# Kernel optimization log

Hardware: AMD Instinct MI355X
Metric: run time of the kernel (lower is better)

The kernel has to match this reference:

```python
import jax, jax.numpy as jnp
import numpy as np

HIDDEN = 32
SEQ = 1440
IN = 11


def lstm_layer(x, Wih, Whh, bih, bhh):
    # x: (B, T, I); PyTorch gate order i, f, g, o stacked along first dim of W (4H, I)
    B, T, _ = x.shape
    H = Whh.shape[1]
    xg = jnp.einsum('bti,gi->btg', x, Wih) + bih + bhh  # (B, T, 4H) input projections precomputed

    def step(carry, xg_t):
        h, c = carry
        g = xg_t + h @ Whh.T  # (B, 4H)
        i, f, gg, o = jnp.split(g, 4, axis=-1)
        i = jax.nn.sigmoid(i)
        f = jax.nn.sigmoid(f)
        gg = jnp.tanh(gg)
        o = jax.nn.sigmoid(o)
        c = f * c + i * gg
        h = o * jnp.tanh(c)
        return (h, c), h

    h0 = jnp.zeros((B, H), x.dtype)
    (_, _), hs = jax.lax.scan(step, (h0, h0), jnp.swapaxes(xg, 0, 1))  # hs: (T, B, H)
    return jnp.swapaxes(hs, 0, 1)


def setup_inputs() -> dict:
    key = jax.random.key(0)
    ks = jax.random.split(key, 14)
    s = 0.1
    return {
        'x': jax.random.normal(ks[0], (1024, IN, SEQ), dtype=jnp.float32),
        'Wih0': jax.random.normal(ks[1], (4 * HIDDEN, IN), dtype=jnp.float32) * s,
        'Whh0': jax.random.normal(ks[2], (4 * HIDDEN, HIDDEN), dtype=jnp.float32) * s,
        'bih0': jax.random.normal(ks[3], (4 * HIDDEN,), dtype=jnp.float32) * s,
        'bhh0': jax.random.normal(ks[4], (4 * HIDDEN,), dtype=jnp.float32) * s,
        'Wih1': jax.random.normal(ks[5], (4 * HIDDEN, HIDDEN), dtype=jnp.float32) * s,
        'Whh1': jax.random.normal(ks[6], (4 * HIDDEN, HIDDEN), dtype=jnp.float32) * s,
        'bih1': jax.random.normal(ks[7], (4 * HIDDEN,), dtype=jnp.float32) * s,
        'bhh1': jax.random.normal(ks[8], (4 * HIDDEN,), dtype=jnp.float32) * s,
        'fc1_w': jax.random.normal(ks[9], (16, HIDDEN), dtype=jnp.float32) * s,
        'fc1_b': jax.random.normal(ks[10], (16,), dtype=jnp.float32) * s,
        'fc2_w': jax.random.normal(ks[11], (1, 16), dtype=jnp.float32) * s,
        'fc2_b': jax.random.normal(ks[12], (1,), dtype=jnp.float32) * s,
    }


def reference(x, Wih0, Whh0, bih0, bhh0, Wih1, Whh1, bih1, bhh1, fc1_w, fc1_b, fc2_w, fc2_b):
    # x.view(-1, 11, 1440).transpose(1, 2) -> (B, 1440, 11)
    xt = jnp.swapaxes(x.reshape(-1, IN, SEQ), 1, 2)
    h1 = lstm_layer(xt, Wih0, Whh0, bih0, bhh0)
    h2 = lstm_layer(h1, Wih1, Whh1, bih1, bhh1)
    out = h2[:, :SEQ - 1, :]  # out[:, -1440:-1, :] with T=1440 -> steps 0..1438
    out = jnp.tanh(out @ fc1_w.T + fc1_b)
    out = out @ fc2_w.T + fc2_b
    return out.squeeze(-1)  # (B, 1439)
```

## Files before the change

### kernel.cpp

```cpp
#include <hip/hip_runtime.h>

#define H    32
#define SEQ  1440
#define NT   (SEQ - 1)
#define INP  11
#define TC   64

__device__ __forceinline__ float rcp_fast(float x) { return __builtin_amdgcn_rcpf(x); }
__device__ __forceinline__ float tanh_f(float x) {
    return fmaf(2.f, rcp_fast(1.f + __expf(-2.f * x)), -1.f);
}

__global__ __launch_bounds__(128, 2)
void lstm_fused_kernel(const float* __restrict__ x,
                       const float* __restrict__ Wih0, const float* __restrict__ Whh0,
                       const float* __restrict__ bih0, const float* __restrict__ bhh0,
                       const float* __restrict__ Wih1, const float* __restrict__ Whh1,
                       const float* __restrict__ bih1, const float* __restrict__ bhh1,
                       const float* __restrict__ fc1w_g, const float* __restrict__ fc1b_g,
                       const float* __restrict__ fc2w_g, const float* __restrict__ fc2b_g,
                       float* __restrict__ out)
{
    __shared__ float h0s[2][H];
    __shared__ float h1s[2][H];
    __shared__ float xs[TC][12];
    __shared__ float h1c[TC][36];

    const int tid  = threadIdx.x;
    const int lane = tid & 63;
    const int wv   = tid >> 6;
    const int m    = lane & 15;
    const int q    = lane >> 4;
    const int jj   = wv * 16 + m;
    const int r    = q * 32 + jj;
    const int b    = blockIdx.x;

    float wih0[12];
    #pragma unroll
    for (int i = 0; i < INP; ++i) wih0[i] = Wih0[r * INP + i];
    wih0[11] = 0.f;
    float whh0[H], wih1[H], whh1[H];
    #pragma unroll
    for (int k = 0; k < H; ++k) {
        whh0[k] = Whh0[r * H + k];
        wih1[k] = Wih1[r * H + k];
        whh1[k] = Whh1[r * H + k];
    }
    const float bs0 = bih0[r] + bhh0[r];
    const float bs1 = bih1[r] + bhh1[r];
    const int   u   = tid & 15;
    float fcw[H];
    #pragma unroll
    for (int k = 0; k < H; ++k) fcw[k] = fc1w_g[u * H + k];
    const float fcb = fc1b_g[u];
    const float f2w = fc2w_g[u];
    const float f2b = fc2b_g[0];

    if (tid < H) { h0s[0][tid] = 0.f; h1s[0][tid] = 0.f; }
    float c0 = 0.f, c1 = 0.f;

    const float* xb   = x   + (size_t)b * INP * SEQ;
    float*       outb = out + (size_t)b * NT;

    __syncthreads();

    for (int cbase = 0; cbase < NT; cbase += TC) {
        const int clen = min(TC, NT - cbase);

        {
            const int col = tid & 63;
            const int r2  = tid >> 6;
            #pragma unroll
            for (int ib = 0; ib < 12; ib += 2) {
                const int row = ib + r2;
                if (row < INP && col < clen)
                    xs[col][row] = xb[row * SEQ + cbase + col];
            }
        }
        __syncthreads();

        for (int tc = 0; tc < clen; ++tc) {
            const int p = (cbase + tc) & 1;

            float act;
            {
                const float4* xv = (const float4*)xs[tc];
                const float4* hv = (const float4*)h0s[p];
                float ax = bs0, a0 = 0.f, a1 = 0.f;
                float4 x0 = xv[0], x1 = xv[1], x2 = xv[2];
                ax = fmaf(wih0[0],  x0.x, ax); ax = fmaf(wih0[1],  x0.y, ax);
                ax = fmaf(wih0[2],  x0.z, ax); ax = fmaf(wih0[3],  x0.w, ax);
                ax = fmaf(wih0[4],  x1.x, ax); ax = fmaf(wih0[5],  x1.y, ax);
                ax = fmaf(wih0[6],  x1.z, ax); ax = fmaf(wih0[7],  x1.w, ax);
                ax = fmaf(wih0[8],  x2.x, ax); ax = fmaf(wih0[9],  x2.y, ax);
                ax = fmaf(wih0[10], x2.z, ax);
                #pragma unroll
                for (int kk = 0; kk < 4; ++kk) {
                    float4 ha = hv[kk], hb = hv[kk + 4];
                    a0 = fmaf(whh0[4*kk+0],    ha.x, a0);
                    a0 = fmaf(whh0[4*kk+1],    ha.y, a0);
                    a0 = fmaf(whh0[4*kk+2],    ha.z, a0);
                    a0 = fmaf(whh0[4*kk+3],    ha.w, a0);
                    a1 = fmaf(whh0[16+4*kk+0], hb.x, a1);
                    a1 = fmaf(whh0[16+4*kk+1], hb.y, a1);
                    a1 = fmaf(whh0[16+4*kk+2], hb.z, a1);
                    a1 = fmaf(whh0[16+4*kk+3], hb.w, a1);
                }
                float a  = (ax + a0) + a1;
                float sc = (q == 2) ? 2.f : 1.f;
                float s  = rcp_fast(1.f + __expf(-sc * a));
                act = (q == 2) ? fmaf(2.f, s, -1.f) : s;
            }
            float gf = __shfl_xor(act, 16);
            float gg = __shfl_xor(act, 32);
            float go = __shfl_xor(act, 48);
            if (q == 0) {
                c0 = fmaf(gf, c0, act * gg);
                h0s[p ^ 1][jj] = go * tanh_f(c0);
            }
            __syncthreads();

            {
                const float4* hav = (const float4*)h0s[p ^ 1];
                const float4* hbv = (const float4*)h1s[p];
                float a0 = bs1, a1 = 0.f, a2 = 0.f, a3 = 0.f;
                #pragma unroll
                for (int kk = 0; kk < 4; ++kk) {
                    float4 ha = hav[kk], ha2 = hav[kk + 4];
                    float4 hb = hbv[kk], hb2 = hbv[kk + 4];
                    a0 = fmaf(wih1[4*kk+0],    ha.x,  a0); a0 = fmaf(wih1[4*kk+1],    ha.y,  a0);
                    a0 = fmaf(wih1[4*kk+2],    ha.z,  a0); a0 = fmaf(wih1[4*kk+3],    ha.w,  a0);
                    a1 = fmaf(wih1[16+4*kk+0], ha2.x, a1); a1 = fmaf(wih1[16+4*kk+1], ha2.y, a1);
                    a1 = fmaf(wih1[16+4*kk+2], ha2.z, a1); a1 = fmaf(wih1[16+4*kk+3], ha2.w, a1);
                    a2 = fmaf(whh1[4*kk+0],    hb.x,  a2); a2 = fmaf(whh1[4*kk+1],    hb.y,  a2);
                    a2 = fmaf(whh1[4*kk+2],    hb.z,  a2); a2 = fmaf(whh1[4*kk+3],    hb.w,  a2);
                    a3 = fmaf(whh1[16+4*kk+0], hb2.x, a3); a3 = fmaf(whh1[16+4*kk+1], hb2.y, a3);
                    a3 = fmaf(whh1[16+4*kk+2], hb2.z, a3); a3 = fmaf(whh1[16+4*kk+3], hb2.w, a3);
                }
                float a  = (a0 + a1) + (a2 + a3);
                float sc = (q == 2) ? 2.f : 1.f;
                float s  = rcp_fast(1.f + __expf(-sc * a));
                act = (q == 2) ? fmaf(2.f, s, -1.f) : s;
            }
            gf = __shfl_xor(act, 16);
            gg = __shfl_xor(act, 32);
            go = __shfl_xor(act, 48);
            if (q == 0) {
                c1 = fmaf(gf, c1, act * gg);
                float hn = go * tanh_f(c1);
                h1s[p ^ 1][jj] = hn;
                h1c[tc][jj]    = hn;
            }
            __syncthreads();
        }

        #pragma unroll
        for (int rep = 0; rep < 8; ++rep) {
            const int tcl = (tid >> 4) + 8 * rep;
            if (tcl < clen) {
                const float4* hv = (const float4*)h1c[tcl];
                float a0 = fcb, a1 = 0.f;
                #pragma unroll
                for (int kk = 0; kk < 4; ++kk) {
                    float4 ha = hv[kk], hb = hv[kk + 4];
                    a0 = fmaf(fcw[4*kk+0],    ha.x, a0); a0 = fmaf(fcw[4*kk+1],    ha.y, a0);
                    a0 = fmaf(fcw[4*kk+2],    ha.z, a0); a0 = fmaf(fcw[4*kk+3],    ha.w, a0);
                    a1 = fmaf(fcw[16+4*kk+0], hb.x, a1); a1 = fmaf(fcw[16+4*kk+1], hb.y, a1);
                    a1 = fmaf(fcw[16+4*kk+2], hb.z, a1); a1 = fmaf(fcw[16+4*kk+3], hb.w, a1);
                }
                float yv = tanh_f(a0 + a1) * f2w;
                yv += __shfl_xor(yv, 1);
                yv += __shfl_xor(yv, 2);
                yv += __shfl_xor(yv, 4);
                yv += __shfl_xor(yv, 8);
                if (u == 0) outb[cbase + tcl] = yv + f2b;
            }
        }
        __syncthreads();
    }
}

extern "C" void kernel_launch(void* const* d_in, const int* in_sizes, int n_in,
                              void* d_out, int out_size, void* d_ws, size_t ws_size,
                              hipStream_t stream)
{
    const float* x    = (const float*)d_in[0];
    const float* Wih0 = (const float*)d_in[1];
    const float* Whh0 = (const float*)d_in[2];
    const float* bih0 = (const float*)d_in[3];
    const float* bhh0 = (const float*)d_in[4];
    const float* Wih1 = (const float*)d_in[5];
    const float* Whh1 = (const float*)d_in[6];
    const float* bih1 = (const float*)d_in[7];
    const float* bhh1 = (const float*)d_in[8];
    const float* fc1w = (const float*)d_in[9];
    const float* fc1b = (const float*)d_in[10];
    const float* fc2w = (const float*)d_in[11];
    const float* fc2b = (const float*)d_in[12];
    float* out = (float*)d_out;

    const int B = in_sizes[0] / (INP * SEQ);
    dim3 grid(B), block(128);
    hipLaunchKernelGGL(lstm_fused_kernel, grid, block, 0, stream,
                       x, Wih0, Whh0, bih0, bhh0, Wih1, Whh1, bih1, bhh1,
                       fc1w, fc1b, fc2w, fc2b, out);
}
```

Measured before the change: 1.308 ms.

## Split gate dot products across lane pairs and gather gates via bpermute

Doubles the block to 256 threads so each gate row's recurrent dot product is split across two lanes and combined with one shuffle. This halves the serial FMA chain on every timestep. Each lane then gathers the i/f/g/o activations with ds_bpermute and computes the cell update redundantly, and one lane per group writes h. The change also folds the tanh scaling into the weights, uses exp2-based sigmoid/tanh, splits the FC head across lane pairs and drops one barrier per chunk. The cost is more waves per block, extra bpermute latency and redundant cell math.

```diff
diff --git a/kernel.cpp b/kernel.cpp
--- a/kernel.cpp
+++ b/kernel.cpp
@@ -6,12 +6,19 @@
 #define INP  11
 #define TC   64
 
-__device__ __forceinline__ float rcp_fast(float x) { return __builtin_amdgcn_rcpf(x); }
+#define LOG2E 1.44269504f
+
+__device__ __forceinline__ float rcp_fast(float x)  { return __builtin_amdgcn_rcpf(x); }
+__device__ __forceinline__ float exp2_fast(float x) { return __builtin_amdgcn_exp2f(x); }
+__device__ __forceinline__ float sigm(float a)      { return rcp_fast(1.f + exp2_fast(a * -LOG2E)); }
 __device__ __forceinline__ float tanh_f(float x) {
-    return fmaf(2.f, rcp_fast(1.f + __expf(-2.f * x)), -1.f);
-}
-
-__global__ __launch_bounds__(128, 2)
+    return fmaf(2.f, rcp_fast(1.f + exp2_fast(x * (-2.f * LOG2E))), -1.f);
+}
+__device__ __forceinline__ float bperm(int byteaddr, float v) {
+    return __int_as_float(__builtin_amdgcn_ds_bpermute(byteaddr, __float_as_int(v)));
+}
+
+__global__ __launch_bounds__(256, 4)
 void lstm_fused_kernel(const float* __restrict__ x,
                        const float* __restrict__ Wih0, const float* __restrict__ Whh0,
                        const float* __restrict__ bih0, const float* __restrict__ bhh0,
@@ -26,35 +33,36 @@
     __shared__ float xs[TC][12];
     __shared__ float h1c[TC][36];
 
-    const int tid  = threadIdx.x;
-    const int lane = tid & 63;
-    const int wv   = tid >> 6;
-    const int m    = lane & 15;
-    const int q    = lane >> 4;
-    const int jj   = wv * 16 + m;
-    const int r    = q * 32 + jj;
-    const int b    = blockIdx.x;
-
-    float wih0[12];
+    const int tid = threadIdx.x;
+    const int l   = tid & 63;
+    const int w   = tid >> 6;
+    const int j   = w * 8 + (l >> 3);
+    const int q   = (l >> 1) & 3;
+    const int kh  = l & 1;
+    const int r   = q * 32 + j;
+    const int ko  = kh * 16;
+    const int b   = blockIdx.x;
+
+    const float gs = (q == 2) ? 2.f : 1.f;
+    const float am = (q == 2) ? 2.f : 1.f;
+    const float ab = (q == 2) ? -1.f : 0.f;
+
+    float wx[12];
     #pragma unroll
-    for (int i = 0; i < INP; ++i) wih0[i] = Wih0[r * INP + i];
-    wih0[11] = 0.f;
-    float whh0[H], wih1[H], whh1[H];
+    for (int i = 0; i < INP; ++i) wx[i] = (kh == 0) ? Wih0[r * INP + i] * gs : 0.f;
+    wx[11] = 0.f;
+    float wh0[16], wi1[16], wh1[16];
     #pragma unroll
-    for (int k = 0; k < H; ++k) {
-        whh0[k] = Whh0[r * H + k];
-        wih1[k] = Wih1[r * H + k];
-        whh1[k] = Whh1[r * H + k];
+    for (int k = 0; k < 16; ++k) {
+        wh0[k] = Whh0[r * H + ko + k] * gs;
+        wi1[k] = Wih1[r * H + ko + k] * gs;
+        wh1[k] = Whh1[r * H + ko + k] * gs;
     }
-    const float bs0 = bih0[r] + bhh0[r];
-    const float bs1 = bih1[r] + bhh1[r];
-    const int   u   = tid & 15;
-    float fcw[H];
-    #pragma unroll
-    for (int k = 0; k < H; ++k) fcw[k] = fc1w_g[u * H + k];
-    const float fcb = fc1b_g[u];
-    const float f2w = fc2w_g[u];
-    const float f2b = fc2b_g[0];
+    const float b0 = (kh == 0) ? (bih0[r] + bhh0[r]) * gs : 0.f;
+    const float b1 = (kh == 0) ? (bih1[r] + bhh1[r]) * gs : 0.f;
+
+    const int lb = (l & 56) | kh;
+    const int ai = (lb | 0) << 2, af = (lb | 2) << 2, ag = (lb | 4) << 2, ao = (lb | 6) << 2;
 
     if (tid < H) { h0s[0][tid] = 0.f; h1s[0][tid] = 0.f; }
     float c0 = 0.f, c1 = 0.f;
@@ -69,12 +77,14 @@
 
         {
             const int col = tid & 63;
-            const int r2  = tid >> 6;
+            const int rw  = tid >> 6;
             #pragma unroll
-            for (int ib = 0; ib < 12; ib += 2) {
-                const int row = ib + r2;
-                if (row < INP && col < clen)
-                    xs[col][row] = xb[row * SEQ + cbase + col];
+            for (int rb = 0; rb < 12; rb += 4) {
+                const int row = rw + rb;
+                if (col < clen) {
+                    if (row < INP)       xs[col][row] = xb[row * SEQ + cbase + col];
+                    else if (row == INP) xs[col][11]  = 0.f;
+                }
             }
         }
         __syncthreads();
@@ -85,98 +95,108 @@
             float act;
             {
                 const float4* xv = (const float4*)xs[tc];
-                const float4* hv = (const float4*)h0s[p];
-                float ax = bs0, a0 = 0.f, a1 = 0.f;
+                const float4* hv = (const float4*)&h0s[p][ko];
+                float a0 = b0, a1 = 0.f;
                 float4 x0 = xv[0], x1 = xv[1], x2 = xv[2];
-                ax = fmaf(wih0[0],  x0.x, ax); ax = fmaf(wih0[1],  x0.y, ax);
-                ax = fmaf(wih0[2],  x0.z, ax); ax = fmaf(wih0[3],  x0.w, ax);
-                ax = fmaf(wih0[4],  x1.x, ax); ax = fmaf(wih0[5],  x1.y, ax);
-                ax = fmaf(wih0[6],  x1.z, ax); ax = fmaf(wih0[7],  x1.w, ax);
-                ax = fmaf(wih0[8],  x2.x, ax); ax = fmaf(wih0[9],  x2.y, ax);
-                ax = fmaf(wih0[10], x2.z, ax);
-                #pragma unroll
-                for (int kk = 0; kk < 4; ++kk) {
-                    float4 ha = hv[kk], hb = hv[kk + 4];
-                    a0 = fmaf(whh0[4*kk+0],    ha.x, a0);
-                    a0 = fmaf(whh0[4*kk+1],    ha.y, a0);
-                    a0 = fmaf(whh0[4*kk+2],    ha.z, a0);
-                    a0 = fmaf(whh0[4*kk+3],    ha.w, a0);
-                    a1 = fmaf(whh0[16+4*kk+0], hb.x, a1);
-                    a1 = fmaf(whh0[16+4*kk+1], hb.y, a1);
-                    a1 = fmaf(whh0[16+4*kk+2], hb.z, a1);
-                    a1 = fmaf(whh0[16+4*kk+3], hb.w, a1);
-                }
-                float a  = (ax + a0) + a1;
-                float sc = (q == 2) ? 2.f : 1.f;
-                float s  = rcp_fast(1.f + __expf(-sc * a));
-                act = (q == 2) ? fmaf(2.f, s, -1.f) : s;
-            }
-            float gf = __shfl_xor(act, 16);
-            float gg = __shfl_xor(act, 32);
-            float go = __shfl_xor(act, 48);
-            if (q == 0) {
-                c0 = fmaf(gf, c0, act * gg);
-                h0s[p ^ 1][jj] = go * tanh_f(c0);
+                a0 = fmaf(wx[0], x0.x, a0);  a1 = fmaf(wx[1], x0.y, a1);
+                a0 = fmaf(wx[2], x0.z, a0);  a1 = fmaf(wx[3], x0.w, a1);
+                a0 = fmaf(wx[4], x1.x, a0);  a1 = fmaf(wx[5], x1.y, a1);
+                a0 = fmaf(wx[6], x1.z, a0);  a1 = fmaf(wx[7], x1.w, a1);
+                a0 = fmaf(wx[8], x2.x, a0);  a1 = fmaf(wx[9], x2.y, a1);
+                a0 = fmaf(wx[10], x2.z, a0);
+                float4 h0 = hv[0], h1v = hv[1], h2v = hv[2], h3v = hv[3];
+                a0 = fmaf(wh0[0],  h0.x,  a0);  a1 = fmaf(wh0[1],  h0.y,  a1);
+                a0 = fmaf(wh0[2],  h0.z,  a0);  a1 = fmaf(wh0[3],  h0.w,  a1);
+                a0 = fmaf(wh0[4],  h1v.x, a0);  a1 = fmaf(wh0[5],  h1v.y, a1);
+                a0 = fmaf(wh0[6],  h1v.z, a0);  a1 = fmaf(wh0[7],  h1v.w, a1);
+                a0 = fmaf(wh0[8],  h2v.x, a0);  a1 = fmaf(wh0[9],  h2v.y, a1);
+                a0 = fmaf(wh0[10], h2v.z, a0);  a1 = fmaf(wh0[11], h2v.w, a1);
+                a0 = fmaf(wh0[12], h3v.x, a0);  a1 = fmaf(wh0[13], h3v.y, a1);
+                a0 = fmaf(wh0[14], h3v.z, a0);  a1 = fmaf(wh0[15], h3v.w, a1);
+                float a = a0 + a1;
+                a += __shfl_xor(a, 1);
+                act = fmaf(am, sigm(a), ab);
+            }
+            {
+                float gi = bperm(ai, act), gf = bperm(af, act);
+                float gg = bperm(ag, act), go = bperm(ao, act);
+                c0 = fmaf(gf, c0, gi * gg);
+                float hn = go * tanh_f(c0);
+                if ((l & 7) == 0) h0s[p ^ 1][j] = hn;
             }
             __syncthreads();
 
             {
-                const float4* hav = (const float4*)h0s[p ^ 1];
-                const float4* hbv = (const float4*)h1s[p];
-                float a0 = bs1, a1 = 0.f, a2 = 0.f, a3 = 0.f;
-                #pragma unroll
-                for (int kk = 0; kk < 4; ++kk) {
-                    float4 ha = hav[kk], ha2 = hav[kk + 4];
-                    float4 hb = hbv[kk], hb2 = hbv[kk + 4];
-                    a0 = fmaf(wih1[4*kk+0],    ha.x,  a0); a0 = fmaf(wih1[4*kk+1],    ha.y,  a0);
-                    a0 = fmaf(wih1[4*kk+2],    ha.z,  a0); a0 = fmaf(wih1[4*kk+3],    ha.w,  a0);
-                    a1 = fmaf(wih1[16+4*kk+0], ha2.x, a1); a1 = fmaf(wih1[16+4*kk+1], ha2.y, a1);
-                    a1 = fmaf(wih1[16+4*kk+2], ha2.z, a1); a1 = fmaf(wih1[16+4*kk+3], ha2.w, a1);
-                    a2 = fmaf(whh1[4*kk+0],    hb.x,  a2); a2 = fmaf(whh1[4*kk+1],    hb.y,  a2);
-                    a2 = fmaf(whh1[4*kk+2],    hb.z,  a2); a2 = fmaf(whh1[4*kk+3],    hb.w,  a2);
-                    a3 = fmaf(whh1[16+4*kk+0], hb2.x, a3); a3 = fmaf(whh1[16+4*kk+1], hb2.y, a3);
-                    a3 = fmaf(whh1[16+4*kk+2], hb2.z, a3); a3 = fmaf(whh1[16+4*kk+3], hb2.w, a3);
-                }
-                float a  = (a0 + a1) + (a2 + a3);
-                float sc = (q == 2) ? 2.f : 1.f;
-                float s  = rcp_fast(1.f + __expf(-sc * a));
-                act = (q == 2) ? fmaf(2.f, s, -1.f) : s;
-            }
-            gf = __shfl_xor(act, 16);
-            gg = __shfl_xor(act, 32);
-            go = __shfl_xor(act, 48);
-            if (q == 0) {
-                c1 = fmaf(gf, c1, act * gg);
+                const float4* iv = (const float4*)&h0s[p ^ 1][ko];
+                const float4* hv = (const float4*)&h1s[p][ko];
+                float a0 = b1, a1 = 0.f, a2 = 0.f, a3 = 0.f;
+                float4 i0 = iv[0], i1 = iv[1], i2 = iv[2], i3 = iv[3];
+                float4 h0v = hv[0], h1v = hv[1], h2v = hv[2], h3v = hv[3];
+                a0 = fmaf(wi1[0],  i0.x,  a0);  a1 = fmaf(wi1[1],  i0.y,  a1);
+                a2 = fmaf(wi1[2],  i0.z,  a2);  a3 = fmaf(wi1[3],  i0.w,  a3);
+                a0 = fmaf(wi1[4],  i1.x,  a0);  a1 = fmaf(wi1[5],  i1.y,  a1);
+                a2 = fmaf(wi1[6],  i1.z,  a2);  a3 = fmaf(wi1[7],  i1.w,  a3);
+                a0 = fmaf(wi1[8],  i2.x,  a0);  a1 = fmaf(wi1[9],  i2.y,  a1);
+                a2 = fmaf(wi1[10], i2.z,  a2);  a3 = fmaf(wi1[11], i2.w,  a3);
+                a0 = fmaf(wi1[12], i3.x,  a0);  a1 = fmaf(wi1[13], i3.y,  a1);
+                a2 = fmaf(wi1[14], i3.z,  a2);  a3 = fmaf(wi1[15], i3.w,  a3);
+                a0 = fmaf(wh1[0],  h0v.x, a0);  a1 = fmaf(wh1[1],  h0v.y, a1);
+                a2 = fmaf(wh1[2],  h0v.z, a2);  a3 = fmaf(wh1[3],  h0v.w, a3);
+                a0 = fmaf(wh1[4],  h1v.x, a0);  a1 = fmaf(wh1[5],  h1v.y, a1);
+                a2 = fmaf(wh1[6],  h1v.z, a2);  a3 = fmaf(wh1[7],  h1v.w, a3);
+                a0 = fmaf(wh1[8],  h2v.x, a0);  a1 = fmaf(wh1[9],  h2v.y, a1);
+                a2 = fmaf(wh1[10], h2v.z, a2);  a3 = fmaf(wh1[11], h2v.w, a3);
+                a0 = fmaf(wh1[12], h3v.x, a0);  a1 = fmaf(wh1[13], h3v.y, a1);
+                a2 = fmaf(wh1[14], h3v.z, a2);  a3 = fmaf(wh1[15], h3v.w, a3);
+                float a = (a0 + a1) + (a2 + a3);
+                a += __shfl_xor(a, 1);
+                act = fmaf(am, sigm(a), ab);
+            }
+            {
+                float gi = bperm(ai, act), gf = bperm(af, act);
+                float gg = bperm(ag, act), go = bperm(ao, act);
+                c1 = fmaf(gf, c1, gi * gg);
                 float hn = go * tanh_f(c1);
-                h1s[p ^ 1][jj] = hn;
-                h1c[tc][jj]    = hn;
+                if ((l & 7) == 0) { h1s[p ^ 1][j] = hn; h1c[tc][j] = hn; }
             }
             __syncthreads();
         }
 
-        #pragma unroll
-        for (int rep = 0; rep < 8; ++rep) {
-            const int tcl = (tid >> 4) + 8 * rep;
-            if (tcl < clen) {
-                const float4* hv = (const float4*)h1c[tcl];
-                float a0 = fcb, a1 = 0.f;
-                #pragma unroll
-                for (int kk = 0; kk < 4; ++kk) {
-                    float4 ha = hv[kk], hb = hv[kk + 4];
-                    a0 = fmaf(fcw[4*kk+0],    ha.x, a0); a0 = fmaf(fcw[4*kk+1],    ha.y, a0);
-                    a0 = fmaf(fcw[4*kk+2],    ha.z, a0); a0 = fmaf(fcw[4*kk+3],    ha.w, a0);
-                    a1 = fmaf(fcw[16+4*kk+0], hb.x, a1); a1 = fmaf(fcw[16+4*kk+1], hb.y, a1);
-                    a1 = fmaf(fcw[16+4*kk+2], hb.z, a1); a1 = fmaf(fcw[16+4*kk+3], hb.w, a1);
+        {
+            const int u   = tid & 15;
+            const int kh2 = (tid >> 4) & 1;
+            const int ti  = tid >> 5;
+            const int ko2 = kh2 * 16;
+            float fw[16];
+            #pragma unroll
+            for (int k = 0; k < 16; ++k) fw[k] = fc1w_g[u * H + ko2 + k];
+            const float fb  = fc1b_g[u];
+            const float f2w = fc2w_g[u];
+            const float f2b = fc2b_g[0];
+            #pragma unroll
+            for (int rep = 0; rep < 8; ++rep) {
+                const int t2 = ti + 8 * rep;
+                if (t2 < clen) {
+                    const float4* hv = (const float4*)&h1c[t2][ko2];
+                    float a0 = 0.f, a1 = 0.f;
+                    float4 v0 = hv[0], v1 = hv[1], v2 = hv[2], v3 = hv[3];
+                    a0 = fmaf(fw[0],  v0.x, a0);  a1 = fmaf(fw[1],  v0.y, a1);
+                    a0 = fmaf(fw[2],  v0.z, a0);  a1 = fmaf(fw[3],  v0.w, a1);
+                    a0 = fmaf(fw[4],  v1.x, a0);  a1 = fmaf(fw[5],  v1.y, a1);
+                    a0 = fmaf(fw[6],  v1.z, a0);  a1 = fmaf(fw[7],  v1.w, a1);
+                    a0 = fmaf(fw[8],  v2.x, a0);  a1 = fmaf(fw[9],  v2.y, a1);
+                    a0 = fmaf(fw[10], v2.z, a0);  a1 = fmaf(fw[11], v2.w, a1);
+                    a0 = fmaf(fw[12], v3.x, a0);  a1 = fmaf(fw[13], v3.y, a1);
+                    a0 = fmaf(fw[14], v3.z, a0);  a1 = fmaf(fw[15], v3.w, a1);
+                    float y = a0 + a1;
+                    y += __shfl_xor(y, 16);
+                    float z = tanh_f(y + fb) * f2w;
+                    z += __shfl_xor(z, 1);  z += __shfl_xor(z, 2);
+                    z += __shfl_xor(z, 4);  z += __shfl_xor(z, 8);
+                    if ((tid & 31) == 0) outb[cbase + t2] = z + f2b;
                 }
-                float yv = tanh_f(a0 + a1) * f2w;
-                yv += __shfl_xor(yv, 1);
-                yv += __shfl_xor(yv, 2);
-                yv += __shfl_xor(yv, 4);
-                yv += __shfl_xor(yv, 8);
-                if (u == 0) outb[cbase + tcl] = yv + f2b;
             }
         }
-        __syncthreads();
     }
 }
 
@@ -200,7 +220,7 @@
     float* out = (float*)d_out;
 
     const int B = in_sizes[0] / (INP * SEQ);
-    dim3 grid(B), block(128);
+    dim3 grid(B), block(256);
     hipLaunchKernelGGL(lstm_fused_kernel, grid, block, 0, stream,
                        x, Wih0, Whh0, bih0, bhh0, Wih1, Whh1, bih1, bhh1,
                        fc1w, fc1b, fc2w, fc2b, out);
```

Result: slower. 1.891 ms (+44.5%).
